# Kernel tuning notes

Measured on AMD Instinct MI355X. Metric: run time of the kernel, lower is better.

The kernel has to match this reference:

```python
import jax, jax.numpy as jnp
import numpy as np

CHANNELS = 512
NUM_HEADS = 8
GROUPS = 32
EPS = 1e-5  # torch GroupNorm default


def setup_inputs() -> dict:
    key = jax.random.key(0)
    ks = jax.random.split(key, 7)
    B, C, H, W = 16, CHANNELS, 64, 64
    x = jax.random.normal(ks[0], (B, C, H, W), dtype=jnp.float32)
    # GroupNorm affine params (torch init: weight=1, bias=0; randomize slightly for a nontrivial baseline)
    gamma = jnp.ones((C,), jnp.float32) + 0.02 * jax.random.normal(ks[1], (C,), jnp.float32)
    beta = 0.02 * jax.random.normal(ks[2], (C,), jnp.float32)
    # 1x1 convs == dense matrices over channel dim
    w_qkv = jax.random.normal(ks[3], (3 * C, C), jnp.float32) / np.sqrt(C)
    b_qkv = 0.01 * jax.random.normal(ks[4], (3 * C,), jnp.float32)
    w_proj = jax.random.normal(ks[5], (C, C), jnp.float32) / np.sqrt(C)
    b_proj = 0.01 * jax.random.normal(ks[6], (C,), jnp.float32)
    return {"x": x, "gamma": gamma, "beta": beta, "w_qkv": w_qkv,
            "b_qkv": b_qkv, "w_proj": w_proj, "b_proj": b_proj}


def _group_norm(x, gamma, beta):
    B, C, H, W = x.shape
    xg = x.reshape(B, GROUPS, C // GROUPS, H, W)
    mean = jnp.mean(xg, axis=(2, 3, 4), keepdims=True)
    var = jnp.mean(jnp.square(xg - mean), axis=(2, 3, 4), keepdims=True)
    xn = ((xg - mean) * jax.lax.rsqrt(var + EPS)).reshape(B, C, H, W)
    return xn * gamma[:, None, None] + beta[:, None, None]


def reference(x, gamma, beta, w_qkv, b_qkv, w_proj, b_proj):
    B, C, H, W = x.shape
    h = NUM_HEADS
    d = C // h  # head_dim
    residual = x
    xn = _group_norm(x, gamma, beta)
    # 1x1 conv == per-pixel dense layer over channels
    qkv = jnp.einsum('bchw,oc->bohw', xn, w_qkv) + b_qkv[:, None, None]
    q, k, v = jnp.split(qkv, 3, axis=1)
    N = H * W
    # rearrange 'b (h c) h1 w1 -> b h c (h1 w1)': rows = head_dim, cols = spatial
    q = q.reshape(B, h, d, N)
    k = k.reshape(B, h, d, N)
    v = v.reshape(B, h, d, N)
    scale = d ** (-0.5)
    # attention over head_dim axis (faithful to the source rearrange)
    attn = jax.nn.softmax(jnp.einsum('bhcn,bhdn->bhcd', q, k) * scale, axis=-1)  # [B,h,d,d]
    out = jnp.einsum('bhcd,bhdn->bhcn', attn, v).reshape(B, C, H, W)
    out = jnp.einsum('bchw,oc->bohw', out, w_proj) + b_proj[:, None, None]
    return out + residual
```

## Files before the change

kernel.cpp:

```cpp
#include <hip/hip_runtime.h>

typedef unsigned short u16;
typedef __attribute__((ext_vector_type(8))) short short8;
typedef __attribute__((ext_vector_type(4))) float floatx4;
typedef __attribute__((ext_vector_type(4))) unsigned int uintx4;

#define B_    16
#define C_    512
#define N_    4096
#define NH_   8
#define HD_   64
#define MQKV  1536
#define NSPL  8

union V16 { uintx4 u; u16 s[8]; short8 h; };

__device__ inline u16 f2bf(float f) {
  union { float f; unsigned int i; } c; c.f = f;
  unsigned int i = c.i;
  return (u16)((i + 0x7FFFu + ((i >> 16) & 1u)) >> 16);
}

__device__ __forceinline__ void gld16(const u16* g, u16* l) {
  __builtin_amdgcn_global_load_lds(
      (const __attribute__((address_space(1))) unsigned int*)g,
      (__attribute__((address_space(3))) unsigned int*)l, 16, 0, 0);
}

__global__ __launch_bounds__(256) void gn_stats(const float* __restrict__ x,
    const float* __restrict__ gamma, const float* __restrict__ beta,
    float* __restrict__ s_arr, float* __restrict__ t_arr) {
  int b = blockIdx.x >> 5, g = blockIdx.x & 31;
  const floatx4* p = (const floatx4*)(x + (size_t)(b * C_ + g * 16) * N_);
  int tid = threadIdx.x;
  float sum = 0.f, ssq = 0.f;
  for (int it = 0; it < 64; ++it) {
    floatx4 v = p[tid + it * 256];
#pragma unroll
    for (int j = 0; j < 4; ++j) { float f = v[j]; sum += f; ssq += f * f; }
  }
#pragma unroll
  for (int off = 32; off > 0; off >>= 1) {
    sum += __shfl_down(sum, off);
    ssq += __shfl_down(ssq, off);
  }
  __shared__ float red[8];
  __shared__ float mv[2];
  int lane = tid & 63, wid = tid >> 6;
  if (lane == 0) { red[wid] = sum; red[wid + 4] = ssq; }
  __syncthreads();
  if (tid == 0) {
    float s = red[0] + red[1] + red[2] + red[3];
    float q = red[4] + red[5] + red[6] + red[7];
    float mean = s * (1.f / 65536.f);
    float var  = q * (1.f / 65536.f) - mean * mean;
    mv[0] = mean; mv[1] = rsqrtf(var + 1e-5f);
  }
  __syncthreads();
  if (tid < 16) {
    int c = g * 16 + tid;
    float ga = gamma[c], be = beta[c];
    float mean = mv[0], rstd = mv[1];
    s_arr[b * C_ + c] = ga * rstd;
    t_arr[b * C_ + c] = be - mean * rstd * ga;
  }
}

__global__ __launch_bounds__(256) void cvt_bf16(const float* __restrict__ src,
                                                u16* __restrict__ dst) {
  int i = blockIdx.x * 256 + threadIdx.x;
  const floatx4* s4 = (const floatx4*)src;
  floatx4 a = s4[2 * i], b = s4[2 * i + 1];
  V16 v;
#pragma unroll
  for (int j = 0; j < 4; ++j) { v.s[j] = f2bf(a[j]); v.s[4 + j] = f2bf(b[j]); }
  ((uintx4*)dst)[i] = v.u;
}

__global__ __launch_bounds__(256) void gn_apply_t(const float* __restrict__ x,
    const float* __restrict__ s_arr, const float* __restrict__ t_arr,
    u16* __restrict__ xt, int b0) {
  __shared__ float T[64][65];
  int bz = blockIdx.z, gb = b0 + bz;
  int n0 = blockIdx.x * 64, c0 = blockIdx.y * 64;
  int tid = threadIdx.x;
  int cl = tid >> 4;
  int nl = (tid & 15) * 4;
  const float* xb = x + (size_t)bz * C_ * N_;
#pragma unroll
  for (int ci = 0; ci < 4; ++ci) {
    int c = c0 + cl + ci * 16;
    float s = s_arr[gb * C_ + c], t = t_arr[gb * C_ + c];
    floatx4 v = *(const floatx4*)(xb + (size_t)c * N_ + n0 + nl);
#pragma unroll
    for (int j = 0; j < 4; ++j) T[cl + ci * 16][nl + j] = s * v[j] + t;
  }
  __syncthreads();
  int n = tid >> 2, cc = (tid & 3) * 16;
  V16 a, b;
#pragma unroll
  for (int j = 0; j < 8; ++j) a.s[j] = f2bf(T[cc + j][n]);
#pragma unroll
  for (int j = 0; j < 8; ++j) b.s[j] = f2bf(T[cc + 8 + j][n]);
  uintx4* dst = (uintx4*)(xt + (size_t)bz * N_ * C_ + (size_t)(n0 + n) * C_ + c0 + cc);
  dst[0] = a.u; dst[1] = b.u;
}

__global__ __launch_bounds__(256) void gemm_bt(
    const u16* __restrict__ A, const u16* __restrict__ Bm,
    const float* __restrict__ bias, const float* __restrict__ resid,
    void* __restrict__ outv, int M, int doRes, int outF32) {
  __shared__ alignas(16) u16 smem[2 * 2 * 128 * 64];
  int bz = blockIdx.z;
  int m0 = blockIdx.y * 128, n0 = blockIdx.x * 128;
  int tid = threadIdx.x, lane = tid & 63, wid = tid >> 6;
  int quad = lane >> 4, l15 = lane & 15;
  int wm = (wid >> 1) * 64, wn = (wid & 1) * 64;
  int sr = tid >> 3, sc = tid & 7;
  const u16* Bb = Bm + (size_t)bz * ((size_t)N_ * C_);
  floatx4 acc[4][4];
#pragma unroll
  for (int i = 0; i < 4; ++i)
#pragma unroll
    for (int j = 0; j < 4; ++j) acc[i][j] = (floatx4)0.f;

  auto stage = [&](int kt, int p) {
    u16* As = smem + p * 16384;
    u16* Bs = As + 8192;
#pragma unroll
    for (int i = 0; i < 4; ++i) {
      int rr = sr + i * 32;
      int cc = sc ^ (rr & 7);
      gld16(A  + (size_t)(m0 + rr) * C_ + kt * 64 + cc * 8, &As[rr * 64 + sc * 8]);
      gld16(Bb + (size_t)(n0 + rr) * C_ + kt * 64 + cc * 8, &Bs[rr * 64 + sc * 8]);
    }
  };

  stage(0, 0);
  asm volatile("s_waitcnt vmcnt(0)" ::: "memory");
  __builtin_amdgcn_s_barrier();
  int cur = 0;
  for (int kt = 0; kt < 8; ++kt) {
    if (kt < 7) stage(kt + 1, cur ^ 1);
    const u16* As = smem + cur * 16384;
    const u16* Bs = As + 8192;
#pragma unroll
    for (int ks = 0; ks < 2; ++ks) {
      short8 af[4], bf8[4];
#pragma unroll
      for (int mi = 0; mi < 4; ++mi) {
        int row = wm + mi * 16 + l15;
        int kc = (ks * 4 + quad) ^ (row & 7);
        af[mi] = *(const short8*)&As[row * 64 + kc * 8];
      }
#pragma unroll
      for (int ni = 0; ni < 4; ++ni) {
        int row = wn + ni * 16 + l15;
        int kc = (ks * 4 + quad) ^ (row & 7);
        bf8[ni] = *(const short8*)&Bs[row * 64 + kc * 8];
      }
#pragma unroll
      for (int mi = 0; mi < 4; ++mi)
#pragma unroll
        for (int ni = 0; ni < 4; ++ni)
          acc[mi][ni] = __builtin_amdgcn_mfma_f32_16x16x32_bf16(af[mi], bf8[ni], acc[mi][ni], 0, 0, 0);
    }
    asm volatile("s_waitcnt vmcnt(0)" ::: "memory");
    __builtin_amdgcn_s_barrier();
    cur ^= 1;
  }
  if (!outF32) {
    u16* E = smem;
#pragma unroll
    for (int mi = 0; mi < 4; ++mi)
#pragma unroll
      for (int ni = 0; ni < 4; ++ni)
#pragma unroll
        for (int r = 0; r < 4; ++r) {
          int row = wm + mi * 16 + quad * 4 + r;
          int col = wn + ni * 16 + l15;
          int ch = col >> 3;
          int cs = (ch & 8) | ((ch & 7) ^ (row & 7));
          E[row * 128 + cs * 8 + (col & 7)] = f2bf(acc[mi][ni][r] + bias[m0 + row]);
        }
    __syncthreads();
    int row = tid >> 1, half = tid & 1;
    u16* orow = (u16*)outv + ((size_t)bz * M + m0 + row) * N_ + n0 + half * 64;
#pragma unroll
    for (int k = 0; k < 8; ++k) {
      int cs = (half * 8) | (k ^ (row & 7));
      *(uintx4*)(orow + k * 8) = *(const uintx4*)&E[row * 128 + cs * 8];
    }
  } else {
    float* E = (float*)smem;
#pragma unroll
    for (int p = 0; p < 2; ++p) {
#pragma unroll
      for (int q = 0; q < 2; ++q)
#pragma unroll
        for (int ni = 0; ni < 4; ++ni)
#pragma unroll
          for (int r = 0; r < 4; ++r) {
            int mi = p * 2 + q;
            int lr = (wid >> 1) * 32 + q * 16 + quad * 4 + r;
            int col = wn + ni * 16 + l15;
            int ch = col >> 2;
            int cs = (ch & ~7) | ((ch & 7) ^ (lr & 7));
            E[lr * 128 + cs * 4 + (col & 3)] =
                acc[mi][ni][r] + bias[m0 + wm + mi * 16 + quad * 4 + r];
          }
      __syncthreads();
      int lr = tid >> 2, qt = tid & 3;
      int o = m0 + (lr >> 5) * 64 + p * 32 + (lr & 31);
      size_t obase = ((size_t)bz * M + o) * N_ + n0 + qt * 4;
#pragma unroll
      for (int k = 0; k < 8; ++k) {
        int ch = k * 4 + qt;
        int cs = (ch & ~7) | ((ch & 7) ^ (lr & 7));
        floatx4 v = *(const floatx4*)&E[lr * 128 + cs * 4];
        if (doRes) v += *(const floatx4*)(resid + obase + (size_t)k * 16);
        *(floatx4*)((float*)outv + obase + (size_t)k * 16) = v;
      }
      if (p == 0) __syncthreads();
    }
  }
}

__global__ __launch_bounds__(256) void qk_partial(const u16* __restrict__ qkv,
    float* __restrict__ spart, int nbh) {
  int h = blockIdx.x, bz = blockIdx.y, p = blockIdx.z;
  const u16* qb = qkv + ((size_t)bz * MQKV + h * HD_) * N_;
  const u16* kb = qkv + ((size_t)bz * MQKV + C_ + h * HD_) * N_;
  int tid = threadIdx.x, lane = tid & 63, wid = tid >> 6;
  int quad = lane >> 4, l15 = lane & 15;
  floatx4 acc[4][4];
#pragma unroll
  for (int i = 0; i < 4; ++i)
#pragma unroll
    for (int j = 0; j < 4; ++j) acc[i][j] = (floatx4)0.f;

  for (int ks = 0; ks < 4; ++ks) {
    int n = p * 512 + wid * 128 + ks * 32 + quad * 8;
    short8 af[4], bf8[4];
#pragma unroll
    for (int mi = 0; mi < 4; ++mi)
      af[mi] = *(const short8*)(qb + (size_t)(mi * 16 + l15) * N_ + n);
#pragma unroll
    for (int ni = 0; ni < 4; ++ni)
      bf8[ni] = *(const short8*)(kb + (size_t)(ni * 16 + l15) * N_ + n);
#pragma unroll
    for (int mi = 0; mi < 4; ++mi)
#pragma unroll
      for (int ni = 0; ni < 4; ++ni)
        acc[mi][ni] = __builtin_amdgcn_mfma_f32_16x16x32_bf16(af[mi], bf8[ni], acc[mi][ni], 0, 0, 0);
  }
  __shared__ float S[64 * 68];
  for (int i = tid; i < 64 * 68; i += 256) S[i] = 0.f;
  __syncthreads();
#pragma unroll
  for (int mi = 0; mi < 4; ++mi)
#pragma unroll
    for (int ni = 0; ni < 4; ++ni)
#pragma unroll
      for (int r = 0; r < 4; ++r)
        atomicAdd(&S[(mi * 16 + quad * 4 + r) * 68 + ni * 16 + l15], acc[mi][ni][r]);
  __syncthreads();
  int bh = bz * NH_ + h;
  float* dst = spart + ((size_t)p * nbh + bh) * 4096 + tid * 16;
  int row = tid >> 2, c0 = (tid & 3) * 16;
#pragma unroll
  for (int j = 0; j < 4; ++j)
    *(floatx4*)(dst + j * 4) = *(const floatx4*)&S[row * 68 + c0 + j * 4];
}

__global__ __launch_bounds__(64) void softmax_rows(const float* __restrict__ spart,
    float* __restrict__ attn, int nbh) {
  int bh = blockIdx.x, c = threadIdx.x;
  const float* sp = spart + (size_t)bh * 4096 + c * 64;
  floatx4 row4[16];
#pragma unroll
  for (int j = 0; j < 16; ++j) row4[j] = *(const floatx4*)(sp + j * 4);
#pragma unroll
  for (int p = 1; p < NSPL; ++p) {
    const float* spp = sp + (size_t)p * nbh * 4096;
#pragma unroll
    for (int j = 0; j < 16; ++j) row4[j] += *(const floatx4*)(spp + j * 4);
  }
  float mx = -1e30f;
#pragma unroll
  for (int j = 0; j < 16; ++j)
#pragma unroll
    for (int e = 0; e < 4; ++e) mx = fmaxf(mx, row4[j][e]);
  float sum = 0.f;
#pragma unroll
  for (int j = 0; j < 16; ++j)
#pragma unroll
    for (int e = 0; e < 4; ++e) {
      float ev = __expf((row4[j][e] - mx) * 0.125f);
      row4[j][e] = ev; sum += ev;
    }
  float inv = 1.f / sum;
  float* dst = attn + (size_t)bh * 4096 + c * 64;
#pragma unroll
  for (int j = 0; j < 16; ++j) *(floatx4*)(dst + j * 4) = row4[j] * inv;
}

__global__ __launch_bounds__(256) void pv_kernel(const float* __restrict__ attn,
    const u16* __restrict__ qkv, u16* __restrict__ ot) {
  int nt = blockIdx.x, h = blockIdx.y, bz = blockIdx.z;
  int n0 = nt * 256;
  const u16* vb = qkv + ((size_t)bz * MQKV + 2 * C_ + h * HD_) * N_;
  __shared__ alignas(16) u16 Ps[64 * 72];
  __shared__ alignas(16) u16 Vs[256 * 72];
  int tid = threadIdx.x, lane = tid & 63, wid = tid >> 6;
  int quad = lane >> 4, l15 = lane & 15;
  const float* ab = attn + (size_t)(bz * NH_ + h) * 4096;
#pragma unroll
  for (int i = 0; i < 16; ++i) {
    int idx = tid + i * 256;
    int row = idx >> 6, col = idx & 63;
    Ps[row * 72 + col] = f2bf(ab[idx]);
  }
#pragma unroll
  for (int i = 0; i < 8; ++i) {
    int l = tid + i * 256;
    int ch = l >> 5, n8 = (l & 31) * 8;
    V16 v; v.u = *(const uintx4*)(vb + (size_t)ch * N_ + n0 + n8);
    int chunk = ch >> 3, clo = ch & 7;
#pragma unroll
    for (int j = 0; j < 8; ++j) {
      int nl = n8 + j;
      Vs[nl * 72 + (chunk ^ ((nl >> 3) & 7)) * 8 + clo] = v.s[j];
    }
  }
  __syncthreads();
  floatx4 acc[4][4];
#pragma unroll
  for (int i = 0; i < 4; ++i)
#pragma unroll
    for (int j = 0; j < 4; ++j) acc[i][j] = (floatx4)0.f;
#pragma unroll
  for (int ks = 0; ks < 2; ++ks) {
    short8 af[4], bf8[4];
    int ko = ks * 32 + quad * 8;
#pragma unroll
    for (int mi = 0; mi < 4; ++mi)
      af[mi] = *(const short8*)&Ps[(mi * 16 + l15) * 72 + ko];
    int chunk = ks * 4 + quad;
#pragma unroll
    for (int ni = 0; ni < 4; ++ni) {
      int nl = wid * 64 + ni * 16 + l15;
      bf8[ni] = *(const short8*)&Vs[nl * 72 + (chunk ^ ((nl >> 3) & 7)) * 8];
    }
#pragma unroll
    for (int mi = 0; mi < 4; ++mi)
#pragma unroll
      for (int ni = 0; ni < 4; ++ni)
        acc[mi][ni] = __builtin_amdgcn_mfma_f32_16x16x32_bf16(af[mi], bf8[ni], acc[mi][ni], 0, 0, 0);
  }
  __syncthreads();
  u16* Ls = Vs;
#pragma unroll
  for (int mi = 0; mi < 4; ++mi)
#pragma unroll
    for (int ni = 0; ni < 4; ++ni)
#pragma unroll
      for (int r = 0; r < 4; ++r) {
        int n  = wid * 64 + ni * 16 + l15;
        int hd = mi * 16 + quad * 4 + r;
        Ls[n * 64 + (((hd >> 3) ^ (n & 7)) * 8) + (hd & 7)] = f2bf(acc[mi][ni][r]);
      }
  __syncthreads();
  uintx4* dst = (uintx4*)(ot + ((size_t)bz * N_ + n0 + tid) * C_ + h * HD_);
#pragma unroll
  for (int k = 0; k < 8; ++k) {
    int kc = k ^ (tid & 7);
    dst[k] = *(const uintx4*)&Ls[tid * 64 + kc * 8];
  }
}

extern "C" void kernel_launch(void* const* d_in, const int* in_sizes, int n_in,
                              void* d_out, int out_size, void* d_ws, size_t ws_size,
                              hipStream_t stream) {
  const float* x      = (const float*)d_in[0];
  const float* gamma  = (const float*)d_in[1];
  const float* beta   = (const float*)d_in[2];
  const float* w_qkv  = (const float*)d_in[3];
  const float* b_qkv  = (const float*)d_in[4];
  const float* w_proj = (const float*)d_in[5];
  const float* b_proj = (const float*)d_in[6];
  float* out = (float*)d_out;

  const size_t fixed = (size_t)2 * B_ * C_ * 4 + (size_t)(MQKV + C_) * C_ * 2;
  const size_t per_batch = (size_t)NH_ * 64 * 64 * 4 + (size_t)N_ * C_ * 2 + (size_t)MQKV * N_ * 2;
  int Bc = 16;
  while (Bc > 1 && fixed + (size_t)Bc * per_batch > ws_size) Bc >>= 1;

  float* s_arr = (float*)d_ws;
  float* t_arr = s_arr + B_ * C_;
  u16* wq = (u16*)(t_arr + B_ * C_);
  u16* wp = wq + MQKV * C_;
  float* attn = (float*)(wp + C_ * C_);
  u16* xt  = (u16*)(attn + (size_t)Bc * NH_ * 64 * 64);
  u16* qkv = xt + (size_t)Bc * N_ * C_;
  float* spart = (float*)xt;

  gn_stats<<<dim3(B_ * 32), dim3(256), 0, stream>>>(x, gamma, beta, s_arr, t_arr);
  cvt_bf16<<<dim3(MQKV * C_ / 2048), dim3(256), 0, stream>>>(w_qkv, wq);
  cvt_bf16<<<dim3(C_ * C_ / 2048), dim3(256), 0, stream>>>(w_proj, wp);

  for (int b0 = 0; b0 < B_; b0 += Bc) {
    int nbh = Bc * NH_;
    gn_apply_t<<<dim3(N_ / 64, C_ / 64, Bc), dim3(256), 0, stream>>>(
        x + (size_t)b0 * C_ * N_, s_arr, t_arr, xt, b0);
    gemm_bt<<<dim3(32, 12, Bc), dim3(256), 0, stream>>>(
        wq, xt, b_qkv, nullptr, qkv, MQKV, 0, 0);
    qk_partial<<<dim3(NH_, Bc, NSPL), dim3(256), 0, stream>>>(qkv, spart, nbh);
    softmax_rows<<<dim3(nbh), dim3(64), 0, stream>>>(spart, attn, nbh);
    pv_kernel<<<dim3(16, NH_, Bc), dim3(256), 0, stream>>>(attn, qkv, xt);
    gemm_bt<<<dim3(32, 4, Bc), dim3(256), 0, stream>>>(
        wp, xt, b_proj, x + (size_t)b0 * C_ * N_, out + (size_t)b0 * C_ * N_, C_, 1, 1);
  }
}
```

Baseline: 679.6 us.

## Use 256x256-tile 512-thread GEMM with split-K pipelining for QKV projection

```diff
diff --git a/kernel.cpp b/kernel.cpp
--- a/kernel.cpp
+++ b/kernel.cpp
@@ -104,6 +104,97 @@
   for (int j = 0; j < 8; ++j) b.s[j] = f2bf(T[cc + 8 + j][n]);
   uintx4* dst = (uintx4*)(xt + (size_t)bz * N_ * C_ + (size_t)(n0 + n) * C_ + c0 + cc);
   dst[0] = a.u; dst[1] = b.u;
+}
+
+__global__ __launch_bounds__(512, 2) void gemm_bt2(
+    const u16* __restrict__ A, const u16* __restrict__ Bm,
+    const float* __restrict__ bias, u16* __restrict__ outp, int M) {
+  __shared__ alignas(16) u16 smem[65536];
+  int bz = blockIdx.z;
+  int m0 = blockIdx.y * 256, n0 = blockIdx.x * 256;
+  int tid = threadIdx.x, lane = tid & 63, wid = tid >> 6;
+  int quad = lane >> 4, l15 = lane & 15;
+  int wm = (wid >> 2) * 128, wn = (wid & 3) * 64;
+  int r0 = tid >> 2, sc = tid & 3;
+  const u16* Bb = Bm + (size_t)bz * ((size_t)N_ * C_);
+  floatx4 acc[8][4];
+#pragma unroll
+  for (int i = 0; i < 8; ++i)
+#pragma unroll
+    for (int j = 0; j < 4; ++j) acc[i][j] = (floatx4)0.f;
+
+  auto stageK = [&](int kt, int ks, int buf) {
+    u16* Adst = smem + buf * 32768 + ks * 8192;
+    u16* Bdst = Adst + 16384;
+    int kb = kt * 64 + ks * 32;
+#pragma unroll
+    for (int ld = 0; ld < 2; ++ld) {
+      int rr = r0 + ld * 128;
+      int cc = sc ^ ((rr >> 1) & 3);
+      gld16(A  + (size_t)(m0 + rr) * C_ + kb + cc * 8, Adst + rr * 32 + sc * 8);
+      gld16(Bb + (size_t)(n0 + rr) * C_ + kb + cc * 8, Bdst + rr * 32 + sc * 8);
+    }
+  };
+  auto computeKS = [&](int ks, int buf) {
+    const u16* As = smem + buf * 32768 + ks * 8192;
+    const u16* Bs = As + 16384;
+    short8 af[8], bf[4];
+#pragma unroll
+    for (int mi = 0; mi < 8; ++mi) {
+      int row = wm + mi * 16 + l15;
+      af[mi] = *(const short8*)&As[row * 32 + (quad ^ ((row >> 1) & 3)) * 8];
+    }
+#pragma unroll
+    for (int ni = 0; ni < 4; ++ni) {
+      int row = wn + ni * 16 + l15;
+      bf[ni] = *(const short8*)&Bs[row * 32 + (quad ^ ((row >> 1) & 3)) * 8];
+    }
+#pragma unroll
+    for (int mi = 0; mi < 8; ++mi)
+#pragma unroll
+      for (int ni = 0; ni < 4; ++ni)
+        acc[mi][ni] = __builtin_amdgcn_mfma_f32_16x16x32_bf16(af[mi], bf[ni], acc[mi][ni], 0, 0, 0);
+  };
+
+  stageK(0, 0, 0);
+  stageK(0, 1, 0);
+  asm volatile("s_waitcnt vmcnt(4)" ::: "memory");
+  __builtin_amdgcn_s_barrier();
+  int cur = 0;
+  for (int kt = 0; kt < 8; ++kt) {
+    if (kt < 7) stageK(kt + 1, 0, cur ^ 1);
+    computeKS(0, cur);
+    if (kt < 7) stageK(kt + 1, 1, cur ^ 1);
+    if (kt < 7) asm volatile("s_waitcnt vmcnt(4)" ::: "memory");
+    else        asm volatile("s_waitcnt vmcnt(0)" ::: "memory");
+    __builtin_amdgcn_s_barrier();
+    computeKS(1, cur);
+    __builtin_amdgcn_s_barrier();
+    cur ^= 1;
+  }
+  __syncthreads();
+  u16* E = smem;
+#pragma unroll
+  for (int mi = 0; mi < 8; ++mi)
+#pragma unroll
+    for (int ni = 0; ni < 4; ++ni)
+#pragma unroll
+      for (int r = 0; r < 4; ++r) {
+        int row = wm + mi * 16 + quad * 4 + r;
+        int col = wn + ni * 16 + l15;
+        int ch = col >> 3;
+        int cs = (ch & ~7) | ((ch & 7) ^ (row & 7));
+        E[row * 256 + cs * 8 + (col & 7)] = f2bf(acc[mi][ni][r] + bias[m0 + row]);
+      }
+  __syncthreads();
+  int row = tid >> 1, half = tid & 1;
+  u16* orow = outp + ((size_t)bz * M + m0 + row) * N_ + n0 + half * 128;
+#pragma unroll
+  for (int k = 0; k < 16; ++k) {
+    int ch = half * 16 + k;
+    int cs = (ch & ~7) | ((ch & 7) ^ (row & 7));
+    *(uintx4*)(orow + k * 8) = *(const uintx4*)&E[row * 256 + cs * 8];
+  }
 }
 
 __global__ __launch_bounds__(256) void gemm_bt(
@@ -413,8 +504,8 @@
     int nbh = Bc * NH_;
     gn_apply_t<<<dim3(N_ / 64, C_ / 64, Bc), dim3(256), 0, stream>>>(
         x + (size_t)b0 * C_ * N_, s_arr, t_arr, xt, b0);
-    gemm_bt<<<dim3(32, 12, Bc), dim3(256), 0, stream>>>(
-        wq, xt, b_qkv, nullptr, qkv, MQKV, 0, 0);
+    gemm_bt2<<<dim3(16, 6, Bc), dim3(512), 0, stream>>>(
+        wq, xt, b_qkv, qkv, MQKV);
     qk_partial<<<dim3(NH_, Bc, NSPL), dim3(256), 0, stream>>>(qkv, spart, nbh);
     softmax_rows<<<dim3(nbh), dim3(64), 0, stream>>>(spart, attn, nbh);
     pv_kernel<<<dim3(16, NH_, Bc), dim3(256), 0, stream>>>(attn, qkv, xt);
```

Measured after the change: 697.0 us. 2.6% more time.

## Fold GroupNorm affine into per-batch QKV weights and fuse stats with transpose

Applied to the files above, without the earlier changes.

```diff
diff --git a/kernel.cpp b/kernel.cpp
--- a/kernel.cpp
+++ b/kernel.cpp
@@ -27,17 +27,37 @@
       (__attribute__((address_space(3))) unsigned int*)l, 16, 0, 0);
 }
 
-__global__ __launch_bounds__(256) void gn_stats(const float* __restrict__ x,
+__global__ __launch_bounds__(256) void gn_stats_t(const float* __restrict__ x,
     const float* __restrict__ gamma, const float* __restrict__ beta,
-    float* __restrict__ s_arr, float* __restrict__ t_arr) {
-  int b = blockIdx.x >> 5, g = blockIdx.x & 31;
-  const floatx4* p = (const floatx4*)(x + (size_t)(b * C_ + g * 16) * N_);
+    float* __restrict__ s_arr, float* __restrict__ t_arr,
+    u16* __restrict__ xtg, int b0) {
+  __shared__ float T[16][256];
+  int bl = blockIdx.x >> 5, g = blockIdx.x & 31;
+  int gb = b0 + bl;
   int tid = threadIdx.x;
+  const float* xb = x + ((size_t)bl * C_ + g * 16) * N_;
+  u16* xd = xtg + ((size_t)bl * 32 + g) * N_ * 16;
   float sum = 0.f, ssq = 0.f;
-  for (int it = 0; it < 64; ++it) {
-    floatx4 v = p[tid + it * 256];
-#pragma unroll
-    for (int j = 0; j < 4; ++j) { float f = v[j]; sum += f; ssq += f * f; }
+  for (int t8 = 0; t8 < 16; ++t8) {
+    int nb = t8 * 256;
+#pragma unroll
+    for (int i = 0; i < 4; ++i) {
+      int idx = tid + i * 256;
+      int row = idx >> 6, col4 = idx & 63;
+      floatx4 v = *(const floatx4*)(xb + (size_t)row * N_ + nb + col4 * 4);
+#pragma unroll
+      for (int j = 0; j < 4; ++j) { float f = v[j]; sum += f; ssq += f * f; }
+      *(floatx4*)&T[row][col4 * 4] = v;
+    }
+    __syncthreads();
+    V16 a, b;
+#pragma unroll
+    for (int j = 0; j < 8; ++j) a.s[j] = f2bf(T[j][tid]);
+#pragma unroll
+    for (int j = 0; j < 8; ++j) b.s[j] = f2bf(T[8 + j][tid]);
+    uintx4* dst = (uintx4*)(xd + (size_t)(nb + tid) * 16);
+    dst[0] = a.u; dst[1] = b.u;
+    __syncthreads();
   }
 #pragma unroll
   for (int off = 32; off > 0; off >>= 1) {
@@ -61,8 +81,8 @@
     int c = g * 16 + tid;
     float ga = gamma[c], be = beta[c];
     float mean = mv[0], rstd = mv[1];
-    s_arr[b * C_ + c] = ga * rstd;
-    t_arr[b * C_ + c] = be - mean * rstd * ga;
+    s_arr[gb * C_ + c] = ga * rstd;
+    t_arr[gb * C_ + c] = be - mean * rstd * ga;
   }
 }
 
@@ -77,39 +97,131 @@
   ((uintx4*)dst)[i] = v.u;
 }
 
-__global__ __launch_bounds__(256) void gn_apply_t(const float* __restrict__ x,
-    const float* __restrict__ s_arr, const float* __restrict__ t_arr,
-    u16* __restrict__ xt, int b0) {
-  __shared__ float T[64][65];
-  int bz = blockIdx.z, gb = b0 + bz;
-  int n0 = blockIdx.x * 64, c0 = blockIdx.y * 64;
-  int tid = threadIdx.x;
-  int cl = tid >> 4;
-  int nl = (tid & 15) * 4;
-  const float* xb = x + (size_t)bz * C_ * N_;
-#pragma unroll
-  for (int ci = 0; ci < 4; ++ci) {
-    int c = c0 + cl + ci * 16;
-    float s = s_arr[gb * C_ + c], t = t_arr[gb * C_ + c];
-    floatx4 v = *(const floatx4*)(xb + (size_t)c * N_ + n0 + nl);
-#pragma unroll
-    for (int j = 0; j < 4; ++j) T[cl + ci * 16][nl + j] = s * v[j] + t;
-  }
-  __syncthreads();
-  int n = tid >> 2, cc = (tid & 3) * 16;
-  V16 a, b;
-#pragma unroll
-  for (int j = 0; j < 8; ++j) a.s[j] = f2bf(T[cc + j][n]);
-#pragma unroll
-  for (int j = 0; j < 8; ++j) b.s[j] = f2bf(T[cc + 8 + j][n]);
-  uintx4* dst = (uintx4*)(xt + (size_t)bz * N_ * C_ + (size_t)(n0 + n) * C_ + c0 + cc);
-  dst[0] = a.u; dst[1] = b.u;
+__global__ __launch_bounds__(256) void fold_w(const float* __restrict__ w_qkv,
+    const float* __restrict__ b_qkv, const float* __restrict__ s_arr,
+    const float* __restrict__ t_arr, u16* __restrict__ wq2,
+    float* __restrict__ bq2, int b0) {
+  int bl = blockIdx.y, gb = b0 + bl;
+  int o = blockIdx.x * 16 + (threadIdx.x >> 4);
+  int cth = threadIdx.x & 15;
+  const float* w  = w_qkv + (size_t)o * C_;
+  const float* sp = s_arr + (size_t)gb * C_;
+  const float* tp = t_arr + (size_t)gb * C_;
+  u16* wd = wq2 + ((size_t)bl * MQKV + o) * C_;
+  V16 buf[4];
+  float bt = 0.f;
+#pragma unroll
+  for (int i = 0; i < 8; ++i) {
+    int c = cth * 32 + i * 4;
+    floatx4 wv = *(const floatx4*)(w + c);
+    floatx4 sv = *(const floatx4*)(sp + c);
+    floatx4 tv = *(const floatx4*)(tp + c);
+#pragma unroll
+    for (int j = 0; j < 4; ++j) {
+      buf[i >> 1].s[(i & 1) * 4 + j] = f2bf(wv[j] * sv[j]);
+      bt += wv[j] * tv[j];
+    }
+  }
+  uintx4* wo = (uintx4*)(wd + cth * 32);
+#pragma unroll
+  for (int i = 0; i < 4; ++i) wo[i] = buf[i].u;
+#pragma unroll
+  for (int off = 8; off > 0; off >>= 1) bt += __shfl_xor(bt, off);
+  if (cth == 0) bq2[(size_t)bl * MQKV + o] = b_qkv[o] + bt;
+}
+
+__global__ __launch_bounds__(256) void gemm_qkv(
+    const u16* __restrict__ Wq, const u16* __restrict__ Xg,
+    const float* __restrict__ bq2, u16* __restrict__ outp, int M) {
+  __shared__ alignas(16) u16 smem[2 * 2 * 128 * 64];
+  int bz = blockIdx.z;
+  int m0 = blockIdx.y * 128, n0 = blockIdx.x * 128;
+  int tid = threadIdx.x, lane = tid & 63, wid = tid >> 6;
+  int quad = lane >> 4, l15 = lane & 15;
+  int wm = (wid >> 1) * 64, wn = (wid & 1) * 64;
+  int sr = tid >> 3, sc = tid & 7;
+  const u16* Ab = Wq + (size_t)bz * ((size_t)M * C_);
+  const u16* Bb = Xg + (size_t)bz * ((size_t)C_ * N_);
+  const float* bias = bq2 + (size_t)bz * M;
+  floatx4 acc[4][4];
+#pragma unroll
+  for (int i = 0; i < 4; ++i)
+#pragma unroll
+    for (int j = 0; j < 4; ++j) acc[i][j] = (floatx4)0.f;
+
+  auto stage = [&](int kt, int p) {
+    u16* As = smem + p * 16384;
+    u16* Bs = As + 8192;
+#pragma unroll
+    for (int i = 0; i < 4; ++i) {
+      int rr = sr + i * 32;
+      int cc = sc ^ (rr & 7);
+      gld16(Ab + (size_t)(m0 + rr) * C_ + kt * 64 + cc * 8, &As[rr * 64 + sc * 8]);
+      gld16(Bb + ((size_t)(kt * 4 + (cc >> 1)) * N_ + n0 + rr) * 16 + (cc & 1) * 8,
+            &Bs[rr * 64 + sc * 8]);
+    }
+  };
+
+  stage(0, 0);
+  asm volatile("s_waitcnt vmcnt(0)" ::: "memory");
+  __builtin_amdgcn_s_barrier();
+  int cur = 0;
+  for (int kt = 0; kt < 8; ++kt) {
+    if (kt < 7) stage(kt + 1, cur ^ 1);
+    const u16* As = smem + cur * 16384;
+    const u16* Bs = As + 8192;
+#pragma unroll
+    for (int ks = 0; ks < 2; ++ks) {
+      short8 af[4], bf8[4];
+#pragma unroll
+      for (int mi = 0; mi < 4; ++mi) {
+        int row = wm + mi * 16 + l15;
+        int kc = (ks * 4 + quad) ^ (row & 7);
+        af[mi] = *(const short8*)&As[row * 64 + kc * 8];
+      }
+#pragma unroll
+      for (int ni = 0; ni < 4; ++ni) {
+        int row = wn + ni * 16 + l15;
+        int kc = (ks * 4 + quad) ^ (row & 7);
+        bf8[ni] = *(const short8*)&Bs[row * 64 + kc * 8];
+      }
+#pragma unroll
+      for (int mi = 0; mi < 4; ++mi)
+#pragma unroll
+        for (int ni = 0; ni < 4; ++ni)
+          acc[mi][ni] = __builtin_amdgcn_mfma_f32_16x16x32_bf16(af[mi], bf8[ni], acc[mi][ni], 0, 0, 0);
+    }
+    asm volatile("s_waitcnt vmcnt(0)" ::: "memory");
+    __builtin_amdgcn_s_barrier();
+    cur ^= 1;
+  }
+  u16* E = smem;
+#pragma unroll
+  for (int mi = 0; mi < 4; ++mi)
+#pragma unroll
+    for (int ni = 0; ni < 4; ++ni)
+#pragma unroll
+      for (int r = 0; r < 4; ++r) {
+        int row = wm + mi * 16 + quad * 4 + r;
+        int col = wn + ni * 16 + l15;
+        int ch = col >> 3;
+        int cs = (ch & 8) | ((ch & 7) ^ (row & 7));
+        E[row * 128 + cs * 8 + (col & 7)] = f2bf(acc[mi][ni][r] + bias[m0 + row]);
+      }
+  __syncthreads();
+  int row = tid >> 1, half = tid & 1;
+  u16* orow = outp + ((size_t)bz * M + m0 + row) * N_ + n0 + half * 64;
+#pragma unroll
+  for (int k = 0; k < 8; ++k) {
+    int cs = (half * 8) | (k ^ (row & 7));
+    *(uintx4*)(orow + k * 8) = *(const uintx4*)&E[row * 128 + cs * 8];
+  }
 }
 
 __global__ __launch_bounds__(256) void gemm_bt(
     const u16* __restrict__ A, const u16* __restrict__ Bm,
     const float* __restrict__ bias, const float* __restrict__ resid,
-    void* __restrict__ outv, int M, int doRes, int outF32) {
+    float* __restrict__ outv, int M) {
   __shared__ alignas(16) u16 smem[2 * 2 * 128 * 64];
   int bz = blockIdx.z;
   int m0 = blockIdx.y * 128, n0 = blockIdx.x * 128;
@@ -169,60 +281,36 @@
     __builtin_amdgcn_s_barrier();
     cur ^= 1;
   }
-  if (!outF32) {
-    u16* E = smem;
-#pragma unroll
-    for (int mi = 0; mi < 4; ++mi)
+  float* E = (float*)smem;
+#pragma unroll
+  for (int p = 0; p < 2; ++p) {
+#pragma unroll
+    for (int q = 0; q < 2; ++q)
 #pragma unroll
       for (int ni = 0; ni < 4; ++ni)
 #pragma unroll
         for (int r = 0; r < 4; ++r) {
-          int row = wm + mi * 16 + quad * 4 + r;
+          int mi = p * 2 + q;
+          int lr = (wid >> 1) * 32 + q * 16 + quad * 4 + r;
           int col = wn + ni * 16 + l15;
-          int ch = col >> 3;
-          int cs = (ch & 8) | ((ch & 7) ^ (row & 7));
-          E[row * 128 + cs * 8 + (col & 7)] = f2bf(acc[mi][ni][r] + bias[m0 + row]);
+          int ch = col >> 2;
+          int cs = (ch & ~7) | ((ch & 7) ^ (lr & 7));
+          E[lr * 128 + cs * 4 + (col & 3)] =
+              acc[mi][ni][r] + bias[m0 + wm + mi * 16 + quad * 4 + r];
         }
     __syncthreads();
-    int row = tid >> 1, half = tid & 1;
-    u16* orow = (u16*)outv + ((size_t)bz * M + m0 + row) * N_ + n0 + half * 64;
+    int lr = tid >> 2, qt = tid & 3;
+    int o = m0 + (lr >> 5) * 64 + p * 32 + (lr & 31);
+    size_t obase = ((size_t)bz * M + o) * N_ + n0 + qt * 4;
 #pragma unroll
     for (int k = 0; k < 8; ++k) {
-      int cs = (half * 8) | (k ^ (row & 7));
-      *(uintx4*)(orow + k * 8) = *(const uintx4*)&E[row * 128 + cs * 8];
-    }
-  } else {
-    float* E = (float*)smem;
-#pragma unroll
-    for (int p = 0; p < 2; ++p) {
-#pragma unroll
-      for (int q = 0; q < 2; ++q)
-#pragma unroll
-        for (int ni = 0; ni < 4; ++ni)
-#pragma unroll
-          for (int r = 0; r < 4; ++r) {
-            int mi = p * 2 + q;
-            int lr = (wid >> 1) * 32 + q * 16 + quad * 4 + r;
-            int col = wn + ni * 16 + l15;
-            int ch = col >> 2;
-            int cs = (ch & ~7) | ((ch & 7) ^ (lr & 7));
-            E[lr * 128 + cs * 4 + (col & 3)] =
-                acc[mi][ni][r] + bias[m0 + wm + mi * 16 + quad * 4 + r];
-          }
-      __syncthreads();
-      int lr = tid >> 2, qt = tid & 3;
-      int o = m0 + (lr >> 5) * 64 + p * 32 + (lr & 31);
-      size_t obase = ((size_t)bz * M + o) * N_ + n0 + qt * 4;
-#pragma unroll
-      for (int k = 0; k < 8; ++k) {
-        int ch = k * 4 + qt;
-        int cs = (ch & ~7) | ((ch & 7) ^ (lr & 7));
-        floatx4 v = *(const floatx4*)&E[lr * 128 + cs * 4];
-        if (doRes) v += *(const floatx4*)(resid + obase + (size_t)k * 16);
-        *(floatx4*)((float*)outv + obase + (size_t)k * 16) = v;
-      }
-      if (p == 0) __syncthreads();
-    }
+      int ch = k * 4 + qt;
+      int cs = (ch & ~7) | ((ch & 7) ^ (lr & 7));
+      floatx4 v = *(const floatx4*)&E[lr * 128 + cs * 4];
+      v += *(const floatx4*)(resid + obase + (size_t)k * 16);
+      *(floatx4*)(outv + obase + (size_t)k * 16) = v;
+    }
+    if (p == 0) __syncthreads();
   }
 }
 
@@ -391,34 +479,38 @@
   const float* b_proj = (const float*)d_in[6];
   float* out = (float*)d_out;
 
-  const size_t fixed = (size_t)2 * B_ * C_ * 4 + (size_t)(MQKV + C_) * C_ * 2;
-  const size_t per_batch = (size_t)NH_ * 64 * 64 * 4 + (size_t)N_ * C_ * 2 + (size_t)MQKV * N_ * 2;
+  const size_t fixed = (size_t)2 * B_ * C_ * 4 + (size_t)C_ * C_ * 2;
+  const size_t per_batch = (size_t)MQKV * 4 + (size_t)MQKV * C_ * 2 +
+                           (size_t)NH_ * 4096 * 4 + (size_t)C_ * N_ * 2 +
+                           (size_t)MQKV * N_ * 2;
   int Bc = 16;
   while (Bc > 1 && fixed + (size_t)Bc * per_batch > ws_size) Bc >>= 1;
 
   float* s_arr = (float*)d_ws;
   float* t_arr = s_arr + B_ * C_;
-  u16* wq = (u16*)(t_arr + B_ * C_);
-  u16* wp = wq + MQKV * C_;
-  float* attn = (float*)(wp + C_ * C_);
-  u16* xt  = (u16*)(attn + (size_t)Bc * NH_ * 64 * 64);
-  u16* qkv = xt + (size_t)Bc * N_ * C_;
-  float* spart = (float*)xt;
-
-  gn_stats<<<dim3(B_ * 32), dim3(256), 0, stream>>>(x, gamma, beta, s_arr, t_arr);
-  cvt_bf16<<<dim3(MQKV * C_ / 2048), dim3(256), 0, stream>>>(w_qkv, wq);
+  u16* wp   = (u16*)(t_arr + B_ * C_);
+  float* bq2 = (float*)(wp + (size_t)C_ * C_);
+  u16* wq2  = (u16*)(bq2 + (size_t)Bc * MQKV);
+  float* attn = (float*)(wq2 + (size_t)Bc * MQKV * C_);
+  u16* xtg  = (u16*)(attn + (size_t)Bc * NH_ * 4096);
+  u16* qkv  = xtg + (size_t)Bc * C_ * N_;
+  float* spart = (float*)xtg;
+  u16* ot = xtg;
+
   cvt_bf16<<<dim3(C_ * C_ / 2048), dim3(256), 0, stream>>>(w_proj, wp);
 
   for (int b0 = 0; b0 < B_; b0 += Bc) {
     int nbh = Bc * NH_;
-    gn_apply_t<<<dim3(N_ / 64, C_ / 64, Bc), dim3(256), 0, stream>>>(
-        x + (size_t)b0 * C_ * N_, s_arr, t_arr, xt, b0);
-    gemm_bt<<<dim3(32, 12, Bc), dim3(256), 0, stream>>>(
-        wq, xt, b_qkv, nullptr, qkv, MQKV, 0, 0);
+    gn_stats_t<<<dim3(Bc * 32), dim3(256), 0, stream>>>(
+        x + (size_t)b0 * C_ * N_, gamma, beta, s_arr, t_arr, xtg, b0);
+    fold_w<<<dim3(MQKV / 16, Bc), dim3(256), 0, stream>>>(
+        w_qkv, b_qkv, s_arr, t_arr, wq2, bq2, b0);
+    gemm_qkv<<<dim3(32, 12, Bc), dim3(256), 0, stream>>>(
+        wq2, xtg, bq2, qkv, MQKV);
     qk_partial<<<dim3(NH_, Bc, NSPL), dim3(256), 0, stream>>>(qkv, spart, nbh);
     softmax_rows<<<dim3(nbh), dim3(64), 0, stream>>>(spart, attn, nbh);
-    pv_kernel<<<dim3(16, NH_, Bc), dim3(256), 0, stream>>>(attn, qkv, xt);
+    pv_kernel<<<dim3(16, NH_, Bc), dim3(256), 0, stream>>>(attn, qkv, ot);
     gemm_bt<<<dim3(32, 4, Bc), dim3(256), 0, stream>>>(
-        wp, xt, b_proj, x + (size_t)b0 * C_ * N_, out + (size_t)b0 * C_ * N_, C_, 1, 1);
-  }
-}
+        wp, ot, b_proj, x + (size_t)b0 * C_ * N_, out + (size_t)b0 * C_ * N_, C_);
+  }
+}
```

Result: no change. 692.4 us (+1.9%).
